# Kernel optimization log

Hardware: AMD Instinct MI355X
Metric: run time of the kernel (lower is better)

The kernel has to match this reference:

```python
import jax, jax.numpy as jnp
import numpy as np
import math

EMBED_DIM = 1024
NUM_HEADS = 16
HEAD_DIM = EMBED_DIM // NUM_HEADS
WINDOW_SIZE = 32  # one-sided; full window = 2*w+1 = 65
SCALING = math.sqrt(HEAD_DIM)


def setup_inputs() -> dict:
    key = jax.random.key(0)
    ks = jax.random.split(key, 9)
    B, S, E = 2, 2048, EMBED_DIM
    s = 1.0 / math.sqrt(E)
    inp = {
        "hidden_states": jax.random.normal(ks[0], (B, S, E), dtype=jnp.float32),
        "q_w": jax.random.uniform(ks[1], (E, E), jnp.float32, -s, s),
        "q_b": jax.random.uniform(ks[2], (E,), jnp.float32, -s, s),
        "k_w": jax.random.uniform(ks[3], (E, E), jnp.float32, -s, s),
        "k_b": jax.random.uniform(ks[4], (E,), jnp.float32, -s, s),
        "v_w": jax.random.uniform(ks[5], (E, E), jnp.float32, -s, s),
        "v_b": jax.random.uniform(ks[6], (E,), jnp.float32, -s, s),
        "o_w": jax.random.uniform(ks[7], (E, E), jnp.float32, -s, s),
        "o_b": jax.random.uniform(ks[8], (E,), jnp.float32, -s, s),
    }
    return inp


def reference(hidden_states, q_w, q_b, k_w, k_b, v_w, v_b, o_w, o_b):
    B, S, E = hidden_states.shape
    H, D, w = NUM_HEADS, HEAD_DIM, WINDOW_SIZE
    W = 2 * w + 1

    q = hidden_states @ q_w.T + q_b
    k = hidden_states @ k_w.T + k_b
    v = hidden_states @ v_w.T + v_b

    # [B, H, S, D]
    q = q.reshape(B, S, H, D).transpose(0, 2, 1, 3)
    k = k.reshape(B, S, H, D).transpose(0, 2, 1, 3)
    v = v.reshape(B, S, H, D).transpose(0, 2, 1, 3)

    # zero-pad seq dim by w on each side (matches F.pad value=0); padded keys
    # contribute score 0 (NOT -inf) exactly like the original unfold scheme.
    k_pad = jnp.pad(k, ((0, 0), (0, 0), (w, w), (0, 0)))
    v_pad = jnp.pad(v, ((0, 0), (0, 0), (w, w), (0, 0)))

    # window gather indices: query i sees padded positions i..i+2w (orig i-w..i+w)
    idx = jnp.arange(S)[:, None] + jnp.arange(W)[None, :]  # [S, W]
    k_slice = k_pad[:, :, idx]  # [B, H, S, W, D]
    v_slice = v_pad[:, :, idx]  # [B, H, S, W, D]

    score = jnp.einsum('bhsd,bhswd->bhsw', q, k_slice) / SCALING
    p = jax.nn.softmax(score, axis=-1)
    attn = jnp.einsum('bhsw,bhswd->bhsd', p, v_slice)

    attn = attn.transpose(0, 2, 1, 3).reshape(B, S, E)
    return attn @ o_w.T + o_b
```

## Files before the change

### kernel.cpp

```cpp
#include <hip/hip_runtime.h>
#include <math.h>

typedef _Float16 h16;
typedef _Float16 h8 __attribute__((ext_vector_type(8)));
typedef float f32x4 __attribute__((ext_vector_type(4)));

__device__ inline void gl2lds16(const void* g, void* l) {
  __builtin_amdgcn_global_load_lds(
      (const __attribute__((address_space(1))) void*)g,
      (__attribute__((address_space(3))) void*)l, 16, 0, 0);
}

__device__ inline void barrier_raw() {
  asm volatile("" ::: "memory");
  __builtin_amdgcn_s_barrier();
  asm volatile("" ::: "memory");
}

#define VMCNT(N) asm volatile("s_waitcnt vmcnt(" #N ")" ::: "memory")
#define LGKM(N) asm volatile("s_waitcnt lgkmcnt(" #N ")" ::: "memory")

__global__ __launch_bounds__(256) void f2h_all(
    const float* __restrict__ hs, const float* __restrict__ w0,
    const float* __restrict__ w1, const float* __restrict__ w2,
    const float* __restrict__ w3, h16* __restrict__ dst, int hsN) {
  int i = (blockIdx.x * 256 + threadIdx.x) * 8;
  const int tot = hsN + 4 * 1048576;
  if (i >= tot) return;
  const float* src;
  int off;
  if (i < hsN) {
    src = hs; off = i;
  } else {
    int k = i - hsN;
    int seg = k >> 20;
    off = k & 1048575;
    src = seg == 0 ? w0 : seg == 1 ? w1 : seg == 2 ? w2 : w3;
  }
  float4 a = *(const float4*)(src + off);
  float4 b = *(const float4*)(src + off + 4);
  h8 o;
  o[0] = (h16)a.x; o[1] = (h16)a.y; o[2] = (h16)a.z; o[3] = (h16)a.w;
  o[4] = (h16)b.x; o[5] = (h16)b.y; o[6] = (h16)b.z; o[7] = (h16)b.w;
  *(h8*)(dst + i) = o;
}

__global__ __launch_bounds__(512, 2) void qkv8(
    const h16* __restrict__ A, const h16* __restrict__ Bw,
    const float* __restrict__ qb, const float* __restrict__ kb,
    const float* __restrict__ vb, h16* __restrict__ qo, h16* __restrict__ ko,
    h16* __restrict__ vo, int nbm, int cpx) {
  __shared__ __align__(16) h16 Asm[2][256][64];
  __shared__ __align__(16) h16 Bsm[2][256][64];

  const int tid = threadIdx.x;
  const int wid = tid >> 6, lane = tid & 63;
  const int lr = lane & 15, lg = lane >> 4;
  const int wr = wid >> 2, wc = wid & 3;
  const int srow = wid * 8 + (lane >> 3);
  const int lsrc = ((lane & 7) ^ (srow & 7)) * 8;

  const int wg = (blockIdx.x % 8) * cpx + blockIdx.x / 8;
  const int bm = wg % nbm, bn = wg / nbm;
  const int row0 = bm * 256, col0 = bn * 256;

  const h16* Ag = A + (size_t)row0 * 1024;
  const h16* Bg = Bw + (size_t)col0 * 1024;

  auto stg = [&](const h16* g, h16* l, int rs) {
    gl2lds16(g + (size_t)(rs + srow) * 1024 + lsrc, l + (rs + wid * 8) * 64);
  };
  auto ldf = [&](const h16* base, int row, int kk) -> h8 {
    return *(const h8*)(base + row * 64 + ((kk * 4 + lg) ^ (lr & 7)) * 8);
  };

  f32x4 acc[8][4] = {};
  h8 bf[4][2], afA[2][2], afB[2][2];

  stg(Ag, &Asm[0][0][0], 0);   stg(Ag, &Asm[0][0][0], 128);
  stg(Bg, &Bsm[0][0][0], 0);   stg(Bg, &Bsm[0][0][0], 64);
  stg(Bg, &Bsm[0][0][0], 128); stg(Bg, &Bsm[0][0][0], 192);
  stg(Ag, &Asm[0][0][0], 64);  stg(Ag, &Asm[0][0][0], 192);
  VMCNT(2);
  barrier_raw();

#define MMA2(AF, M0)                                                           \
  __builtin_amdgcn_s_setprio(1);                                               \
  _Pragma("unroll") for (int kk = 0; kk < 2; ++kk)                             \
      _Pragma("unroll") for (int mi = 0; mi < 2; ++mi)                         \
          _Pragma("unroll") for (int n = 0; n < 4; ++n)                        \
              acc[(M0) + mi][n] = __builtin_amdgcn_mfma_f32_16x16x32_f16(      \
                  AF[mi][kk], bf[n][kk], acc[(M0) + mi][n], 0, 0, 0);          \
  __builtin_amdgcn_s_setprio(0)

#define TILE_PHASES(T, RBUF, WBUF)                                             \
  {                                                                            \
    const h16* Ar = &Asm[RBUF][0][0];                                          \
    const h16* Br = &Bsm[RBUF][0][0];                                          \
    h16* Aw = &Asm[WBUF][0][0];                                                \
    h16* Bwl = &Bsm[WBUF][0][0];                                               \
    const h16* Agt = Ag + (size_t)((T) + 1) * 64;                              \
    const h16* Bgt = Bg + (size_t)((T) + 1) * 64;                              \
    const bool st = (T) < 15;                                                  \
                             \
    _Pragma("unroll") for (int n = 0; n < 4; ++n) {                            \
      bf[n][0] = ldf(Br, wc * 64 + n * 16 + lr, 0);                            \
      bf[n][1] = ldf(Br, wc * 64 + n * 16 + lr, 1);                            \
    }                                                                          \
    _Pragma("unroll") for (int kk = 0; kk < 2; ++kk) {                         \
      afA[0][kk] = ldf(Ar, wr * 128 + 0 * 16 + lr, kk);                        \
      afA[1][kk] = ldf(Ar, wr * 128 + 1 * 16 + lr, kk);                        \
    }                                                                          \
    _Pragma("unroll") for (int kk = 0; kk < 2; ++kk) {                         \
      afB[0][kk] = ldf(Ar, wr * 128 + 2 * 16 + lr, kk);                        \
      afB[1][kk] = ldf(Ar, wr * 128 + 3 * 16 + lr, kk);                        \
    }                                                                          \
    if (st) { stg(Agt, Aw, 0); stg(Agt, Aw, 128); }                            \
    barrier_raw();                                                             \
    LGKM(4);                                                                   \
    MMA2(afA, 0);                                                              \
    if (st) { VMCNT(2); } else { VMCNT(0); }                                   \
    barrier_raw();                                                             \
                                         \
    _Pragma("unroll") for (int kk = 0; kk < 2; ++kk) {                         \
      afA[0][kk] = ldf(Ar, wr * 128 + 4 * 16 + lr, kk);                        \
      afA[1][kk] = ldf(Ar, wr * 128 + 5 * 16 + lr, kk);                        \
    }                                                                          \
    if (st) { stg(Bgt, Bwl, 0); stg(Bgt, Bwl, 64); }                           \
    barrier_raw();                                                             \
    LGKM(4);                                                                   \
    MMA2(afB, 2);                                                              \
    barrier_raw();                                                             \
                                         \
    _Pragma("unroll") for (int kk = 0; kk < 2; ++kk) {                         \
      afB[0][kk] = ldf(Ar, wr * 128 + 6 * 16 + lr, kk);                        \
      afB[1][kk] = ldf(Ar, wr * 128 + 7 * 16 + lr, kk);                        \
    }                                                                          \
    if (st) { stg(Bgt, Bwl, 128); stg(Bgt, Bwl, 192); }                        \
    barrier_raw();                                                             \
    LGKM(4);                                                                   \
    MMA2(afA, 4);                                                              \
    barrier_raw();                                                             \
                                          \
    if (st) { stg(Agt, Aw, 64); stg(Agt, Aw, 192); }                           \
    barrier_raw();                                                             \
    LGKM(0);                                                                   \
    MMA2(afB, 6);                                                              \
    if (st) { VMCNT(2); } else { VMCNT(0); }                                   \
    barrier_raw();                                                             \
  }

  for (int tt = 0; tt < 16; tt += 2) {
    TILE_PHASES(tt, 0, 1);
    TILE_PHASES(tt + 1, 1, 0);
  }
#undef TILE_PHASES
#undef MMA2

  const int tsel = col0 >> 10;
  const float* bp = tsel == 0 ? qb : (tsel == 1 ? kb : vb);
  h16* outp = tsel == 0 ? qo : (tsel == 1 ? ko : vo);
#pragma unroll
  for (int n = 0; n < 4; ++n) {
    const int cidx = col0 + wc * 64 + n * 16 + lr;
    const int jj = cidx & 1023;
    const float bv = bp[jj];
    const int hh = jj >> 6, dd = jj & 63;
#pragma unroll
    for (int m = 0; m < 8; ++m) {
#pragma unroll
      for (int j = 0; j < 4; ++j) {
        const int r = row0 + wr * 128 + m * 16 + lg * 4 + j;
        const int bb = r >> 11, ss = r & 2047;
        outp[(((size_t)bb * 16 + hh) * 2048 + ss) * 64 + dd] =
            (h16)(acc[m][n][j] + bv);
      }
    }
  }
}

__global__ __launch_bounds__(256) void gemm_o(
    const h16* __restrict__ A, const h16* __restrict__ Bw,
    const float* __restrict__ b0, float* __restrict__ Cf, int M, int N, int K) {
  __shared__ __align__(16) h16 Ash[128 * 32];
  __shared__ __align__(16) h16 Bsh[128 * 32];
  const int tid = threadIdx.x;
  const int wave = tid >> 6, lane = tid & 63;
  const int lr = lane & 15, lg = lane >> 4;
  const int wr = wave >> 1, wc = wave & 1;
  const int row0 = blockIdx.x * 128, col0 = blockIdx.y * 128;

  f32x4 acc[4][4] = {};

  const int nk = K >> 5;
  for (int kt = 0; kt < nk; ++kt) {
#pragma unroll
    for (int i = 0; i < 2; ++i) {
      const int grp = wave * 2 + i;
      const int c = grp * 64 + lane;
      const int r = c >> 2, cc = c & 3;
      gl2lds16(A + (size_t)(row0 + r) * K + kt * 32 + cc * 8, &Ash[grp * 512]);
      gl2lds16(Bw + (size_t)(col0 + r) * K + kt * 32 + cc * 8, &Bsh[grp * 512]);
    }
    __syncthreads();
    h8 af[4], bf[4];
#pragma unroll
    for (int m = 0; m < 4; ++m)
      af[m] = *(const h8*)&Ash[(wr * 64 + m * 16 + lr) * 32 + lg * 8];
#pragma unroll
    for (int n = 0; n < 4; ++n)
      bf[n] = *(const h8*)&Bsh[(wc * 64 + n * 16 + lr) * 32 + lg * 8];
#pragma unroll
    for (int m = 0; m < 4; ++m)
#pragma unroll
      for (int n = 0; n < 4; ++n)
        acc[m][n] =
            __builtin_amdgcn_mfma_f32_16x16x32_f16(af[m], bf[n], acc[m][n], 0, 0, 0);
    __syncthreads();
  }

#pragma unroll
  for (int m = 0; m < 4; ++m)
#pragma unroll
    for (int n = 0; n < 4; ++n)
#pragma unroll
      for (int j = 0; j < 4; ++j) {
        const int r = row0 + wr * 64 + m * 16 + lg * 4 + j;
        const int cidx = col0 + wc * 64 + n * 16 + lr;
        Cf[(size_t)r * N + cidx] = acc[m][n][j] + b0[cidx];
      }
}

__global__ __launch_bounds__(256) void swattn(const h16* __restrict__ Q,
                                              const h16* __restrict__ K,
                                              const h16* __restrict__ V,
                                              h16* __restrict__ O) {
  __shared__ __align__(16) h16 Ksh[128 * 72];
  __shared__ __align__(16) h16 Vsh[64 * 136];
  __shared__ __align__(16) h16 Psh[4][16 * 136];

  const int qb0 = blockIdx.x * 64;
  const int bh = blockIdx.y;
  const int b = bh >> 4, h = bh & 15;
  const int tid = threadIdx.x;
  const int wave = tid >> 6, lane = tid & 63;
  const int lr = lane & 15, lg = lane >> 4;

  const h16* Qb = Q + (size_t)bh * 2048 * 64;
  const h16* Kb = K + (size_t)bh * 2048 * 64;
  const h16* Vb = V + (size_t)bh * 2048 * 64;

#pragma unroll
  for (int i = 0; i < 4; ++i) {
    const int c = tid * 4 + i;
    const int row = c >> 3, c8 = c & 7;
    const int t = qb0 - 32 + row;
    h8 kv, vv;
    if (t >= 0 && t < 2048) {
      kv = *(const h8*)&Kb[(size_t)t * 64 + c8 * 8];
      vv = *(const h8*)&Vb[(size_t)t * 64 + c8 * 8];
    } else {
#pragma unroll
      for (int j = 0; j < 8; ++j) { kv[j] = (h16)0.f; vv[j] = (h16)0.f; }
    }
    *(h8*)&Ksh[row * 72 + c8 * 8] = kv;
#pragma unroll
    for (int j = 0; j < 8; ++j) Vsh[(c8 * 8 + j) * 136 + row] = vv[j];
  }
  __syncthreads();

  const int qrow = qb0 + wave * 16 + lr;
  h8 qa[2];
#pragma unroll
  for (int kk = 0; kk < 2; ++kk)
    qa[kk] = *(const h8*)&Qb[(size_t)qrow * 64 + kk * 32 + lg * 8];

  f32x4 sacc[8] = {};
#pragma unroll
  for (int n = 0; n < 8; ++n)
#pragma unroll
    for (int kk = 0; kk < 2; ++kk) {
      h8 kb = *(const h8*)&Ksh[(n * 16 + lr) * 72 + kk * 32 + lg * 8];
      sacc[n] = __builtin_amdgcn_mfma_f32_16x16x32_f16(qa[kk], kb, sacc[n], 0, 0, 0);
    }

  float p[8][4];
#pragma unroll
  for (int j = 0; j < 4; ++j) {
    const int wrow = wave * 16 + lg * 4 + j;
    float mx = -1e30f;
#pragma unroll
    for (int n = 0; n < 8; ++n) {
      const int d = n * 16 + lr - wrow;
      float s = (d < 0 || d > 64) ? -1e30f : sacc[n][j] * 0.125f;
      p[n][j] = s;
      mx = fmaxf(mx, s);
    }
#pragma unroll
    for (int off = 1; off < 16; off <<= 1) mx = fmaxf(mx, __shfl_xor(mx, off, 64));
    float sum = 0.f;
#pragma unroll
    for (int n = 0; n < 8; ++n) {
      const float e = __expf(p[n][j] - mx);
      p[n][j] = e;
      sum += e;
    }
#pragma unroll
    for (int off = 1; off < 16; off <<= 1) sum += __shfl_xor(sum, off, 64);
    const float inv = 1.f / sum;
#pragma unroll
    for (int n = 0; n < 8; ++n) p[n][j] *= inv;
  }

#pragma unroll
  for (int n = 0; n < 8; ++n)
#pragma unroll
    for (int j = 0; j < 4; ++j)
      Psh[wave][(lg * 4 + j) * 136 + n * 16 + lr] = (h16)p[n][j];
  __syncthreads();

  f32x4 oacc[4] = {};
#pragma unroll
  for (int kk = 0; kk < 4; ++kk) {
    h8 pa = *(const h8*)&Psh[wave][lr * 136 + kk * 32 + lg * 8];
#pragma unroll
    for (int n = 0; n < 4; ++n) {
      h8 vb = *(const h8*)&Vsh[(n * 16 + lr) * 136 + kk * 32 + lg * 8];
      oacc[n] = __builtin_amdgcn_mfma_f32_16x16x32_f16(pa, vb, oacc[n], 0, 0, 0);
    }
  }

#pragma unroll
  for (int n = 0; n < 4; ++n)
#pragma unroll
    for (int j = 0; j < 4; ++j) {
      const int s = qb0 + wave * 16 + lg * 4 + j;
      const int d = n * 16 + lr;
      O[((size_t)b * 2048 + s) * 1024 + h * 64 + d] = (h16)oacc[n][j];
    }
}

extern "C" void kernel_launch(void* const* d_in, const int* in_sizes, int n_in,
                              void* d_out, int out_size, void* d_ws, size_t ws_size,
                              hipStream_t stream) {
  const float* hs = (const float*)d_in[0];
  const float* qw = (const float*)d_in[1];
  const float* qb = (const float*)d_in[2];
  const float* kw = (const float*)d_in[3];
  const float* kb = (const float*)d_in[4];
  const float* vw = (const float*)d_in[5];
  const float* vb = (const float*)d_in[6];
  const float* ow = (const float*)d_in[7];
  const float* ob = (const float*)d_in[8];

  const int M = in_sizes[0] / 1024;

  h16* hsH = (h16*)d_ws;
  h16* wqkv = hsH + (size_t)M * 1024;
  h16* woH = wqkv + (size_t)3072 * 1024;
  h16* qH = woH + (size_t)1024 * 1024;
  h16* kH = qH + (size_t)M * 1024;
  h16* vH = kH + (size_t)M * 1024;
  h16* attnH = vH + (size_t)M * 1024;

  const int tot = M * 1024 + 4 * 1048576;
  f2h_all<<<(tot / 8 + 255) / 256, 256, 0, stream>>>(hs, qw, kw, vw, ow, hsH,
                                                     M * 1024);

  const int nbm = M / 256;
  const int nwg = nbm * 12;
  qkv8<<<nwg, 512, 0, stream>>>(hsH, wqkv, qb, kb, vb, qH, kH, vH, nbm, nwg / 8);

  swattn<<<dim3(32, M / 2048 * 16), 256, 0, stream>>>(qH, kH, vH, attnH);

  gemm_o<<<dim3(M / 128, 8), 256, 0, stream>>>(attnH, woH, ob, (float*)d_out, M,
                                               1024, 1024);
}
```

Baseline: 91.64 us.

## Replace output projection GEMM with single-wave double-buffered swizzled kernel

Replaces the 256-thread output-projection GEMM (128x128 tiles, BK=32, single-buffered with two syncthreads per step) with a one-wave kernel computing 32x128 tiles at BK=64. Global-to-LDS loads are double-buffered and ordered with vmcnt waits instead of barriers, use an XOR-swizzled LDS layout to avoid bank conflicts, and remap block indices for locality. This yields 1024 small workgroups instead of 256, which should fill the CUs better and remove barrier stalls. The cost is more redundant reads of the weight matrix per output row and hardcoded 1024 dimensions.

New measurement: 86.81 us. -5.3%, faster.

```diff
diff --git a/kernel.cpp b/kernel.cpp
--- a/kernel.cpp
+++ b/kernel.cpp
@@ -102,7 +102,6 @@
     const h16* Agt = Ag + (size_t)((T) + 1) * 64;                              \
     const h16* Bgt = Bg + (size_t)((T) + 1) * 64;                              \
     const bool st = (T) < 15;                                                  \
-                             \
     _Pragma("unroll") for (int n = 0; n < 4; ++n) {                            \
       bf[n][0] = ldf(Br, wc * 64 + n * 16 + lr, 0);                            \
       bf[n][1] = ldf(Br, wc * 64 + n * 16 + lr, 1);                            \
@@ -121,7 +120,6 @@
     MMA2(afA, 0);                                                              \
     if (st) { VMCNT(2); } else { VMCNT(0); }                                   \
     barrier_raw();                                                             \
-                                         \
     _Pragma("unroll") for (int kk = 0; kk < 2; ++kk) {                         \
       afA[0][kk] = ldf(Ar, wr * 128 + 4 * 16 + lr, kk);                        \
       afA[1][kk] = ldf(Ar, wr * 128 + 5 * 16 + lr, kk);                        \
@@ -131,7 +129,6 @@
     LGKM(4);                                                                   \
     MMA2(afB, 2);                                                              \
     barrier_raw();                                                             \
-                                         \
     _Pragma("unroll") for (int kk = 0; kk < 2; ++kk) {                         \
       afB[0][kk] = ldf(Ar, wr * 128 + 6 * 16 + lr, kk);                        \
       afB[1][kk] = ldf(Ar, wr * 128 + 7 * 16 + lr, kk);                        \
@@ -141,7 +138,6 @@
     LGKM(4);                                                                   \
     MMA2(afA, 4);                                                              \
     barrier_raw();                                                             \
-                                          \
     if (st) { stg(Agt, Aw, 64); stg(Agt, Aw, 192); }                           \
     barrier_raw();                                                             \
     LGKM(0);                                                                   \
@@ -179,56 +175,83 @@
   }
 }
 
-__global__ __launch_bounds__(256) void gemm_o(
-    const h16* __restrict__ A, const h16* __restrict__ Bw,
-    const float* __restrict__ b0, float* __restrict__ Cf, int M, int N, int K) {
-  __shared__ __align__(16) h16 Ash[128 * 32];
-  __shared__ __align__(16) h16 Bsh[128 * 32];
-  const int tid = threadIdx.x;
-  const int wave = tid >> 6, lane = tid & 63;
+__global__ __launch_bounds__(64) void oproj1w(const h16* __restrict__ A,
+                                              const h16* __restrict__ Bw,
+                                              const float* __restrict__ b0,
+                                              float* __restrict__ Cf) {
+  __shared__ __align__(16) h16 Ash[2][32][64];
+  __shared__ __align__(16) h16 Bsh[2][128][64];
+
+  const int lane = threadIdx.x;
   const int lr = lane & 15, lg = lane >> 4;
-  const int wr = wave >> 1, wc = wave & 1;
-  const int row0 = blockIdx.x * 128, col0 = blockIdx.y * 128;
-
-  f32x4 acc[4][4] = {};
-
-  const int nk = K >> 5;
-  for (int kt = 0; kt < nk; ++kt) {
-#pragma unroll
-    for (int i = 0; i < 2; ++i) {
-      const int grp = wave * 2 + i;
-      const int c = grp * 64 + lane;
-      const int r = c >> 2, cc = c & 3;
-      gl2lds16(A + (size_t)(row0 + r) * K + kt * 32 + cc * 8, &Ash[grp * 512]);
-      gl2lds16(Bw + (size_t)(col0 + r) * K + kt * 32 + cc * 8, &Bsh[grp * 512]);
-    }
-    __syncthreads();
-    h8 af[4], bf[4];
-#pragma unroll
-    for (int m = 0; m < 4; ++m)
-      af[m] = *(const h8*)&Ash[(wr * 64 + m * 16 + lr) * 32 + lg * 8];
-#pragma unroll
-    for (int n = 0; n < 4; ++n)
-      bf[n] = *(const h8*)&Bsh[(wc * 64 + n * 16 + lr) * 32 + lg * 8];
-#pragma unroll
-    for (int m = 0; m < 4; ++m)
-#pragma unroll
-      for (int n = 0; n < 4; ++n)
-        acc[m][n] =
-            __builtin_amdgcn_mfma_f32_16x16x32_f16(af[m], bf[n], acc[m][n], 0, 0, 0);
-    __syncthreads();
-  }
-
-#pragma unroll
-  for (int m = 0; m < 4; ++m)
-#pragma unroll
-    for (int n = 0; n < 4; ++n)
+  const int srw = lane >> 3;
+  const int csw = ((lane & 7) ^ (srw & 7)) * 8;
+
+  const int wg = (blockIdx.x & 7) * 128 + (blockIdx.x >> 3);
+  const int bm = wg & 127, bn = wg >> 7;
+  const int row0 = bm * 32, col0 = bn * 128;
+
+  const h16* Ag = A + (size_t)row0 * 1024;
+  const h16* Bg = Bw + (size_t)col0 * 1024;
+
+  auto stage = [&](int t, int bi) {
+    const int kof = t * 64 + csw;
+#pragma unroll
+    for (int rs = 0; rs < 32; rs += 8)
+      gl2lds16(Ag + (size_t)(rs + srw) * 1024 + kof, &Ash[bi][rs][0]);
+#pragma unroll
+    for (int rs = 0; rs < 128; rs += 8)
+      gl2lds16(Bg + (size_t)(rs + srw) * 1024 + kof, &Bsh[bi][rs][0]);
+  };
+  auto ldf = [&](const h16* base, int row, int kk) -> h8 {
+    return *(const h8*)(base + row * 64 + ((kk * 4 + lg) ^ (row & 7)) * 8);
+  };
+
+  f32x4 acc[2][8] = {};
+
+  stage(0, 0);
+  for (int t = 0; t < 16; ++t) {
+    if (t + 1 < 16) {
+      stage(t + 1, (t + 1) & 1);
+      VMCNT(20);
+    } else {
+      VMCNT(0);
+    }
+    const h16* Ar = &Ash[t & 1][0][0];
+    const h16* Br = &Bsh[t & 1][0][0];
+    h8 af[2][2], bf[8][2];
+#pragma unroll
+    for (int m = 0; m < 2; ++m)
+#pragma unroll
+      for (int kk = 0; kk < 2; ++kk) af[m][kk] = ldf(Ar, m * 16 + lr, kk);
+#pragma unroll
+    for (int n = 0; n < 8; ++n)
+#pragma unroll
+      for (int kk = 0; kk < 2; ++kk) bf[n][kk] = ldf(Br, n * 16 + lr, kk);
+    __builtin_amdgcn_s_setprio(1);
+#pragma unroll
+    for (int m = 0; m < 2; ++m)
+#pragma unroll
+      for (int n = 0; n < 8; ++n)
+#pragma unroll
+        for (int kk = 0; kk < 2; ++kk)
+          acc[m][n] = __builtin_amdgcn_mfma_f32_16x16x32_f16(af[m][kk], bf[n][kk],
+                                                             acc[m][n], 0, 0, 0);
+    __builtin_amdgcn_s_setprio(0);
+  }
+
+#pragma unroll
+  for (int n = 0; n < 8; ++n) {
+    const int cidx = col0 + n * 16 + lr;
+    const float bv = b0[cidx];
+#pragma unroll
+    for (int m = 0; m < 2; ++m)
 #pragma unroll
       for (int j = 0; j < 4; ++j) {
-        const int r = row0 + wr * 64 + m * 16 + lg * 4 + j;
-        const int cidx = col0 + wc * 64 + n * 16 + lr;
-        Cf[(size_t)r * N + cidx] = acc[m][n][j] + b0[cidx];
+        const int r = row0 + m * 16 + lg * 4 + j;
+        Cf[(size_t)r * 1024 + cidx] = acc[m][n][j] + bv;
       }
+  }
 }
 
 __global__ __launch_bounds__(256) void swattn(const h16* __restrict__ Q,
@@ -373,6 +396,5 @@
 
   swattn<<<dim3(32, M / 2048 * 16), 256, 0, stream>>>(qH, kH, vH, attnH);
 
-  gemm_o<<<dim3(M / 128, 8), 256, 0, stream>>>(attnH, woH, ob, (float*)d_out, M,
-                                               1024, 1024);
-}
+  oproj1w<<<1024, 64, 0, stream>>>(attnH, woH, ob, (float*)d_out);
+}
```
